# Kernel tuning notes

Measured on AMD Instinct MI355X. Metric: run time of the kernel, lower is better.

The kernel has to match this reference:

```python
import jax, jax.numpy as jnp
import numpy as np

B, N, T, D, H, L, N_HOP = 8, 512, 64, 256, 256, 2, 1
NEG = -1e18


def setup_inputs() -> dict:
    key = jax.random.key(0)
    ks = jax.random.split(key, 16)
    sc = 0.05
    return {
        "attn_mem": jax.random.normal(ks[0], (B, N, D), jnp.float32),
        "mem_sizes": jax.random.randint(ks[1], (B,), 1, N + 1).astype(jnp.int32),
        "lstm_in": jax.random.normal(ks[2], (B, T, D), jnp.float32),
        "init_h": jax.random.uniform(ks[3], (L, H), jnp.float32, -0.01, 0.01),
        "init_c": jax.random.uniform(ks[4], (L, H), jnp.float32, -0.01, 0.01),
        "init_i": jax.random.uniform(ks[5], (D,), jnp.float32, -0.1, 0.1),
        # stacked LSTM weights (layer0 input dim D == H so stacking is valid)
        "w_ih": jax.random.normal(ks[6], (L, 4 * H, D), jnp.float32) * sc,
        "w_hh": jax.random.normal(ks[7], (L, 4 * H, H), jnp.float32) * sc,
        "b_ih": jnp.zeros((L, 4 * H), jnp.float32),
        "b_hh": jnp.zeros((L, 4 * H), jnp.float32),
        "attn_wm": jax.random.normal(ks[8], (D, H), jnp.float32) * sc,
        "attn_wq": jax.random.normal(ks[9], (H, H), jnp.float32) * sc,
        "attn_v": jax.random.uniform(ks[10], (H,), jnp.float32, -0.01, 0.01),
        "hop_wm": jax.random.normal(ks[11], (D, H), jnp.float32) * sc,
        "hop_wq": jax.random.normal(ks[12], (H, H), jnp.float32) * sc,
        "hop_v": jax.random.uniform(ks[13], (H,), jnp.float32, -0.01, 0.01),
    }


def _additive_score(feat, query, v, wq):
    # feat: [B,N,H]  query: [B,S,H]  ->  score: [B,S,N]
    q = query @ wq  # [B,S,H]
    s = jnp.tanh(feat[:, None, :, :] + q[:, :, None, :])  # [B,S,N,H] (large)
    return jnp.einsum("bsnh,h->bsn", s, v)


def _run_lstm(x, h0, c0, w_ih, w_hh, b_ih, b_hh):
    # x: [S,B,D] time-major; PyTorch gate order i,f,g,o
    n_layer = h0.shape[0]

    def step(carry, x_t):
        h, c = carry
        inp = x_t
        hs, cs = [], []
        for l in range(n_layer):
            g = inp @ w_ih[l].T + h[l] @ w_hh[l].T + b_ih[l] + b_hh[l]
            i_g, f_g, g_g, o_g = jnp.split(g, 4, axis=-1)
            c_n = jax.nn.sigmoid(f_g) * c[l] + jax.nn.sigmoid(i_g) * jnp.tanh(g_g)
            h_n = jax.nn.sigmoid(o_g) * jnp.tanh(c_n)
            hs.append(h_n)
            cs.append(c_n)
            inp = h_n
        return (jnp.stack(hs), jnp.stack(cs)), inp

    _, ys = jax.lax.scan(step, (h0, c0), x)
    return ys  # [S,B,H]


def reference(attn_mem, mem_sizes, lstm_in, init_h, init_c, init_i,
              w_ih, w_hh, b_ih, b_hh,
              attn_wm, attn_wq, attn_v, hop_wm, hop_wq, hop_v):
    bs, n_mem, _ = attn_mem.shape
    attn_feat = attn_mem @ attn_wm  # [B,N,H]
    hop_feat = attn_mem @ hop_wm    # [B,N,H]

    h0 = jnp.broadcast_to(init_h[:, None, :], (init_h.shape[0], bs, init_h.shape[1]))
    c0 = jnp.broadcast_to(init_c[:, None, :], h0.shape)
    seq = jnp.concatenate(
        [jnp.broadcast_to(init_i[None, None, :], (bs, 1, init_i.shape[0])), lstm_in],
        axis=1,
    )  # [B,T+1,D]
    query = _run_lstm(seq.transpose(1, 0, 2), h0, c0, w_ih, w_hh, b_ih, b_hh)
    query = query.transpose(1, 0, 2)  # [B,T+1,H]

    valid = jnp.arange(n_mem)[None, None, :] < mem_sizes[:, None, None]  # [B,1,N]
    for _ in range(N_HOP):
        score = _additive_score(hop_feat, query, hop_v, hop_wq)  # [B,T+1,N]
        score = jnp.where(valid, score, NEG)
        norm = jax.nn.softmax(score, axis=-1)
        query = jnp.einsum("bsn,bnh->bsh", norm, hop_feat)

    return _additive_score(attn_feat, query, attn_v, attn_wq)  # [B,T+1,N]
```

## Files before the change

### kernel.cpp

```cpp
#include <hip/hip_runtime.h>

#define BB 8
#define NN 512
#define TT 64
#define SS 65
#define DD 256
#define HH 256
#define G4 1024

__device__ __forceinline__ float fsigmoid(float x) {
    return __builtin_amdgcn_rcpf(1.f + __expf(-x));
}
__device__ __forceinline__ float ftanh(float x) {
    float e = __expf(2.f * x);
    return fmaf(-2.f, __builtin_amdgcn_rcpf(e + 1.f), 1.f);
}

__global__ void __launch_bounds__(256) pre_kernel(
    const float* __restrict__ lstm_in, const float* __restrict__ init_i,
    const float* __restrict__ init_h, const float* __restrict__ w_ih,
    const float* __restrict__ b_ih, const float* __restrict__ b_hh,
    float* __restrict__ xg0,
    const float* __restrict__ attn_mem, const float* __restrict__ attn_wm,
    const float* __restrict__ hop_wm,
    float* __restrict__ attn_feat, float* __restrict__ hop_feat,
    unsigned long long* __restrict__ S0, unsigned long long* __restrict__ S1)
{
    const int tid = threadIdx.x;
    const int blk = blockIdx.x;
    if (blk >= 400) {
        int i = (blk - 400) * 256 + tid;
        if (i < 2048) {
            S0[i] = (1ULL << 32) | (unsigned long long)(unsigned)__float_as_uint(init_h[i & 255]);
        } else if (i < 4096) {
            S1[i - 2048] = (1ULL << 32)
                         | (unsigned long long)(unsigned)__float_as_uint(init_h[HH + (i & 255)]);
        } else if (i < 4096 + 65 * 2048) {
            S0[2048 + (i - 4096)] = 0ULL;
        } else if (i < 4096 + 130 * 2048) {
            S1[2048 + (i - (4096 + 65 * 2048))] = 0ULL;
        }
        return;
    }
    __shared__ __align__(16) float smem[3264];
    const int tm = (tid >> 4) * 4, tn = (tid & 15) * 4;
    const int arow = tid >> 2, akq = (tid & 3) << 2;

    if (blk < 144) {
        float* As = smem;
        float* Bs = smem + 1088;
        const int bm = (blk % 9) * 64, bn = (blk / 9) * 64;
        float acc[4][4] = {};
        for (int k0 = 0; k0 < 256; k0 += 16) {
            {
                int m = bm + arow;
                float4 v = make_float4(0.f, 0.f, 0.f, 0.f);
                if (m < 520) {
                    int s = m % 65, b = m / 65;
                    const float* src = (s == 0) ? (init_i + k0 + akq)
                        : (lstm_in + ((size_t)b * TT + (s - 1)) * DD + k0 + akq);
                    v = *(const float4*)src;
                }
                As[(akq + 0) * 68 + arow] = v.x; As[(akq + 1) * 68 + arow] = v.y;
                As[(akq + 2) * 68 + arow] = v.z; As[(akq + 3) * 68 + arow] = v.w;
            }
            {
                int n = bn + arow;
                float4 v = *(const float4*)(w_ih + (size_t)n * 256 + k0 + akq);
                Bs[(akq + 0) * 68 + (n - bn)] = v.x; Bs[(akq + 1) * 68 + (n - bn)] = v.y;
                Bs[(akq + 2) * 68 + (n - bn)] = v.z; Bs[(akq + 3) * 68 + (n - bn)] = v.w;
            }
            __syncthreads();
#pragma unroll
            for (int kk = 0; kk < 16; ++kk) {
                float4 a = *(const float4*)&As[kk * 68 + tm];
                float4 b = *(const float4*)&Bs[kk * 68 + tn];
                float av[4] = {a.x, a.y, a.z, a.w};
                float bv[4] = {b.x, b.y, b.z, b.w};
#pragma unroll
                for (int i = 0; i < 4; ++i)
#pragma unroll
                    for (int jj = 0; jj < 4; ++jj)
                        acc[i][jj] = fmaf(av[i], bv[jj], acc[i][jj]);
            }
            __syncthreads();
        }
        float bad[4];
#pragma unroll
        for (int jj = 0; jj < 4; ++jj)
            bad[jj] = b_ih[bn + tn + jj] + b_hh[bn + tn + jj];
#pragma unroll
        for (int i = 0; i < 4; ++i) {
            int m = bm + tm + i;
            if (m < 520)
                *(float4*)(xg0 + (size_t)m * 1024 + bn + tn) =
                    make_float4(acc[i][0] + bad[0], acc[i][1] + bad[1],
                                acc[i][2] + bad[2], acc[i][3] + bad[3]);
        }
    } else {
        float* As  = smem;
        float* Bs  = smem + 1088;
        float* Bs2 = smem + 2176;
        const int tileid = blk - 144;
        const int bm = (tileid & 63) * 64, bn = (tileid >> 6) * 64;
        float acc1[4][4] = {}, acc2[4][4] = {};
        for (int k0 = 0; k0 < 256; k0 += 16) {
            float4 va = *(const float4*)(attn_mem + (size_t)(bm + arow) * 256 + k0 + akq);
            As[(akq + 0) * 68 + arow] = va.x; As[(akq + 1) * 68 + arow] = va.y;
            As[(akq + 2) * 68 + arow] = va.z; As[(akq + 3) * 68 + arow] = va.w;
            int kk = tid >> 4, nq = (tid & 15) << 2;
            *(float4*)&Bs[kk * 68 + nq]  = *(const float4*)(attn_wm + (size_t)(k0 + kk) * 256 + bn + nq);
            *(float4*)&Bs2[kk * 68 + nq] = *(const float4*)(hop_wm  + (size_t)(k0 + kk) * 256 + bn + nq);
            __syncthreads();
#pragma unroll
            for (int kk2 = 0; kk2 < 16; ++kk2) {
                float4 a  = *(const float4*)&As[kk2 * 68 + tm];
                float4 b1 = *(const float4*)&Bs[kk2 * 68 + tn];
                float4 b2 = *(const float4*)&Bs2[kk2 * 68 + tn];
                float av[4] = {a.x, a.y, a.z, a.w};
                float b1v[4] = {b1.x, b1.y, b1.z, b1.w};
                float b2v[4] = {b2.x, b2.y, b2.z, b2.w};
#pragma unroll
                for (int i = 0; i < 4; ++i)
#pragma unroll
                    for (int jj = 0; jj < 4; ++jj) {
                        acc1[i][jj] = fmaf(av[i], b1v[jj], acc1[i][jj]);
                        acc2[i][jj] = fmaf(av[i], b2v[jj], acc2[i][jj]);
                    }
            }
            __syncthreads();
        }
#pragma unroll
        for (int i = 0; i < 4; ++i) {
            int m = bm + tm + i;
            *(float4*)(attn_feat + (size_t)m * 256 + bn + tn) =
                make_float4(acc1[i][0], acc1[i][1], acc1[i][2], acc1[i][3]);
            *(float4*)(hop_feat + (size_t)m * 256 + bn + tn) =
                make_float4(acc2[i][0], acc2[i][1], acc2[i][2], acc2[i][3]);
        }
    }
}

__device__ __forceinline__ float dot16(const float4* w, const float* hp) {
    float4 s = make_float4(0.f, 0.f, 0.f, 0.f);
#pragma unroll
    for (int k = 0; k < 16; ++k) {
        float4 h4 = *(const float4*)(hp + 4 * k);
        s.x = fmaf(w[k].x, h4.x, s.x);
        s.y = fmaf(w[k].y, h4.y, s.y);
        s.z = fmaf(w[k].z, h4.z, s.z);
        s.w = fmaf(w[k].w, h4.w, s.w);
    }
    return (s.x + s.y) + (s.z + s.w);
}

__device__ __forceinline__ float poll_h(const unsigned long long* p, unsigned want) {
    unsigned long long u = __hip_atomic_load(p, __ATOMIC_RELAXED, __HIP_MEMORY_SCOPE_AGENT);
    while ((unsigned)(u >> 32) != want) {
        u = __hip_atomic_load(p, __ATOMIC_RELAXED, __HIP_MEMORY_SCOPE_AGENT);
    }
    return __uint_as_float((unsigned)u);
}

__global__ void __launch_bounds__(1024, 4) lstm_kernel(
    const float* __restrict__ w_ih, const float* __restrict__ w_hh,
    const float* __restrict__ b_ih, const float* __restrict__ b_hh,
    const float* __restrict__ xg0, const float* __restrict__ init_c,
    unsigned long long* __restrict__ S0, unsigned long long* __restrict__ S1,
    float* __restrict__ query)
{
    __shared__ float hls[64 * 68];
    __shared__ float part[1024];
    const int tid = threadIdx.x;
    const int blk = blockIdx.x;
    const int g = tid * 2;
    const int sb = g >> 8, r0 = g & 255, sg0 = r0 >> 6, kq = r0 & 63;
    float* const dst = &hls[(sg0 * 8 + sb) * 68 + kq];

    if (blk < 32) {
        const int jl = tid & 7, gate = (tid >> 3) & 3, b = (tid >> 5) & 7, seg = tid >> 8;
        const int j0 = blk * 8, j = j0 + jl;
        float4 w[16];
        {
            const float4* wr = (const float4*)(w_hh + (size_t)(gate * HH + j) * HH + seg * 64);
#pragma unroll
            for (int k = 0; k < 16; ++k) w[k] = wr[k];
        }
        const int fj = tid >> 3, fb = tid & 7;
        float creg = (tid < 64) ? init_c[j0 + fj] : 0.f;
        const int chunk = seg * 8 + b;
        const int pidx = (chunk * 8 + jl) * 4 + gate;

        for (int t = 0; t < SS; ++t) {
            float xg[4];
            if (tid < 64) {
                const float* xp = xg0 + ((size_t)fb * SS + t) * G4 + (j0 + fj);
#pragma unroll
                for (int gg = 0; gg < 4; ++gg) xg[gg] = xp[gg * 256];
            }
            {
                const unsigned long long* src = S0 + (size_t)t * 2048 + g;
                dst[0] = poll_h(src, (unsigned)(t + 1));
                dst[1] = poll_h(src + 1, (unsigned)(t + 1));
            }
            __syncthreads();
            part[pidx] = dot16(w, &hls[chunk * 68]);
            __syncthreads();
            if (tid < 64) {
                float g0 = xg[0], g1 = xg[1], g2 = xg[2], g3 = xg[3];
#pragma unroll
                for (int s2 = 0; s2 < 4; ++s2) {
                    const float* pp = &part[((s2 * 8 + fb) * 8 + fj) * 4];
                    g0 += pp[0]; g1 += pp[1]; g2 += pp[2]; g3 += pp[3];
                }
                float c = fsigmoid(g1) * creg + fsigmoid(g0) * ftanh(g2);
                float h = fsigmoid(g3) * ftanh(c);
                creg = c;
                unsigned long long u = ((unsigned long long)(unsigned)(t + 2) << 32)
                                     | (unsigned long long)(unsigned)__float_as_uint(h);
                __hip_atomic_store(S0 + (size_t)(t + 1) * 2048 + fb * 256 + (j0 + fj), u,
                                   __ATOMIC_RELAXED, __HIP_MEMORY_SCOPE_AGENT);
            }
        }
    } else {
        const int jl = tid & 3, gate = (tid >> 2) & 3, b = (tid >> 4) & 7, seg = tid >> 7;
        const int j0 = (blk - 32) * 4, j = j0 + jl;
        float4 w[16];
        {
            const float* base = (seg < 4)
                ? (w_ih + (size_t)(G4 + gate * HH + j) * HH + seg * 64)
                : (w_hh + (size_t)(G4 + gate * HH + j) * HH + (seg - 4) * 64);
            const float4* wr = (const float4*)base;
#pragma unroll
            for (int k = 0; k < 16; ++k) w[k] = wr[k];
        }
        const int fj = tid >> 3, fb = tid & 7;
        float creg = 0.f, bias[4] = {0.f, 0.f, 0.f, 0.f};
        if (tid < 32) {
            creg = init_c[HH + j0 + fj];
#pragma unroll
            for (int gg = 0; gg < 4; ++gg)
                bias[gg] = b_ih[G4 + gg * HH + j0 + fj] + b_hh[G4 + gg * HH + j0 + fj];
        }
        const int chunk = seg * 8 + b;
        const int pidx = chunk * 16 + jl * 4 + gate;

        for (int t = 0; t < SS; ++t) {
            {
                const unsigned long long* src = S0 + (size_t)(t + 1) * 2048 + g;
                dst[0] = poll_h(src, (unsigned)(t + 2));
                dst[1] = poll_h(src + 1, (unsigned)(t + 2));
            }
            __syncthreads();
            if (seg < 4) part[pidx] = dot16(w, &hls[chunk * 68]);
            {
                const unsigned long long* src = S1 + (size_t)t * 2048 + g;
                float v0 = poll_h(src, (unsigned)(t + 1));
                float v1 = poll_h(src + 1, (unsigned)(t + 1));
                dst[32 * 68 + 0] = v0;
                dst[32 * 68 + 1] = v1;
            }
            __syncthreads();
            if (seg >= 4) part[pidx] = dot16(w, &hls[chunk * 68]);
            __syncthreads();
            if (tid < 32) {
                float g0 = bias[0], g1 = bias[1], g2 = bias[2], g3 = bias[3];
#pragma unroll
                for (int s2 = 0; s2 < 8; ++s2) {
                    const float* pp = &part[(s2 * 8 + fb) * 16 + fj * 4];
                    g0 += pp[0]; g1 += pp[1]; g2 += pp[2]; g3 += pp[3];
                }
                float c = fsigmoid(g1) * creg + fsigmoid(g0) * ftanh(g2);
                float h = fsigmoid(g3) * ftanh(c);
                creg = c;
                int jj = j0 + fj;
                unsigned long long u = ((unsigned long long)(unsigned)(t + 2) << 32)
                                     | (unsigned long long)(unsigned)__float_as_uint(h);
                __hip_atomic_store(S1 + (size_t)(t + 1) * 2048 + fb * 256 + jj, u,
                                   __ATOMIC_RELAXED, __HIP_MEMORY_SCOPE_AGENT);
                query[((size_t)fb * SS + t) * HH + jj] = h;
            }
        }
    }
}

__global__ void __launch_bounds__(512) score_kernel(
    const float* __restrict__ qin, const float* __restrict__ wq,
    const float* __restrict__ feat, const float* __restrict__ v,
    const int* __restrict__ mem_sizes, float* __restrict__ out, int masked)
{
    const int s = blockIdx.x, b = blockIdx.y, tid = threadIdx.x;
    __shared__ float qrow[256], vs[256];
    __shared__ float partm[512];
    if (tid < 256) qrow[tid] = qin[((size_t)b * SS + s) * HH + tid];
    else           vs[tid - 256] = v[tid - 256];
    __syncthreads();
    {
        const int kh = tid >> 8, hp2 = tid & 255;
        const float* wp = wq + (size_t)(kh * 128) * HH + hp2;
        const float* qr = qrow + kh * 128;
        float a = 0.f;
#pragma unroll 8
        for (int hh = 0; hh < 128; ++hh) a = fmaf(qr[hh], wp[(size_t)hh * HH], a);
        partm[tid] = a;
    }
    __syncthreads();
    if (tid < 256) qrow[tid] = partm[tid] + partm[tid + 256];
    __syncthreads();

    const int msize = masked ? mem_sizes[b] : NN;
    const int lane = tid & 63, wv = tid >> 6;
    float* ob = out + ((size_t)b * SS + s) * NN;
    for (int n = msize + tid; n < NN; n += 512) ob[n] = -1e18f;
    float4 q4 = *(const float4*)&qrow[lane << 2];
    float4 v4 = *(const float4*)&vs[lane << 2];
    const float* fb = feat + (size_t)b * NN * HH + (lane << 2);
    int n = wv;
    for (; n + 8 < msize; n += 16) {
        float4 fa = *(const float4*)(fb + (size_t)n * HH);
        float4 fc = *(const float4*)(fb + (size_t)(n + 8) * HH);
        float a0 = ftanh(fa.x + q4.x) * v4.x + ftanh(fa.y + q4.y) * v4.y
                 + ftanh(fa.z + q4.z) * v4.z + ftanh(fa.w + q4.w) * v4.w;
        float a1 = ftanh(fc.x + q4.x) * v4.x + ftanh(fc.y + q4.y) * v4.y
                 + ftanh(fc.z + q4.z) * v4.z + ftanh(fc.w + q4.w) * v4.w;
#pragma unroll
        for (int off = 32; off; off >>= 1) {
            a0 += __shfl_xor(a0, off, 64);
            a1 += __shfl_xor(a1, off, 64);
        }
        if (lane == 0) { ob[n] = a0; ob[n + 8] = a1; }
    }
    for (; n < msize; n += 8) {
        float4 fa = *(const float4*)(fb + (size_t)n * HH);
        float a0 = ftanh(fa.x + q4.x) * v4.x + ftanh(fa.y + q4.y) * v4.y
                 + ftanh(fa.z + q4.z) * v4.z + ftanh(fa.w + q4.w) * v4.w;
#pragma unroll
        for (int off = 32; off; off >>= 1) a0 += __shfl_xor(a0, off, 64);
        if (lane == 0) ob[n] = a0;
    }
}

__global__ void __launch_bounds__(512) swsum8_kernel(
    const float* __restrict__ sc, const float* __restrict__ feat,
    const int* __restrict__ mem_sizes, float* __restrict__ q2raw)
{
    const int st = blockIdx.x, b = blockIdx.y, tid = threadIdx.x;
    const int s0 = st * 5;
    const int msize = mem_sizes[b];
    __shared__ float pls[5 * 520];
    __shared__ float partw[8 * 5 * 256];
    for (int i = tid; i < 5 * 512; i += 512) {
        int s = i >> 9, n = i & 511;
        pls[s * 520 + n] = (n < msize)
            ? sc[((size_t)b * SS + s0 + s) * NN + n] : -3e38f;
    }
    __syncthreads();
    const int lane = tid & 63, wv = tid >> 6;
    if (wv < 5) {
        const int r = wv;
        float x[8];
        float m = -3e38f;
#pragma unroll
        for (int k = 0; k < 8; ++k) {
            x[k] = pls[r * 520 + lane + 64 * k];
            m = fmaxf(m, x[k]);
        }
#pragma unroll
        for (int off = 32; off; off >>= 1) m = fmaxf(m, __shfl_xor(m, off, 64));
        float l = 0.f;
#pragma unroll
        for (int k = 0; k < 8; ++k) { x[k] = __expf(x[k] - m); l += x[k]; }
#pragma unroll
        for (int off = 32; off; off >>= 1) l += __shfl_xor(l, off, 64);
        float inv = __builtin_amdgcn_rcpf(l);
#pragma unroll
        for (int k = 0; k < 8; ++k) pls[r * 520 + lane + 64 * k] = x[k] * inv;
    }
    __syncthreads();
    {
        float4 acc[5];
#pragma unroll
        for (int s = 0; s < 5; ++s) acc[s] = make_float4(0.f, 0.f, 0.f, 0.f);
        const float* fb = feat + (size_t)b * NN * HH + (lane << 2);
        const int nb = wv * 64;
        for (int i = 0; i < 64; ++i) {
            float4 f = *(const float4*)(fb + (size_t)(nb + i) * HH);
#pragma unroll
            for (int s = 0; s < 5; ++s) {
                float p = pls[s * 520 + nb + i];
                acc[s].x = fmaf(p, f.x, acc[s].x);
                acc[s].y = fmaf(p, f.y, acc[s].y);
                acc[s].z = fmaf(p, f.z, acc[s].z);
                acc[s].w = fmaf(p, f.w, acc[s].w);
            }
        }
#pragma unroll
        for (int s = 0; s < 5; ++s)
            *(float4*)&partw[(wv * 5 + s) * 256 + (lane << 2)] = acc[s];
    }
    __syncthreads();
    for (int i = tid; i < 5 * 256; i += 512) {
        int s = i >> 8, h = i & 255;
        float r = 0.f;
#pragma unroll
        for (int w = 0; w < 8; ++w) r += partw[(w * 5 + s) * 256 + h];
        q2raw[((size_t)b * SS + s0 + s) * HH + h] = r;
    }
}

extern "C" void kernel_launch(void* const* d_in, const int* in_sizes, int n_in,
                              void* d_out, int out_size, void* d_ws, size_t ws_size,
                              hipStream_t stream) {
    const float* attn_mem  = (const float*)d_in[0];
    const int*   mem_sizes = (const int*)d_in[1];
    const float* lstm_in   = (const float*)d_in[2];
    const float* init_h    = (const float*)d_in[3];
    const float* init_c    = (const float*)d_in[4];
    const float* init_i    = (const float*)d_in[5];
    const float* w_ih      = (const float*)d_in[6];
    const float* w_hh      = (const float*)d_in[7];
    const float* b_ih      = (const float*)d_in[8];
    const float* b_hh      = (const float*)d_in[9];
    const float* attn_wm   = (const float*)d_in[10];
    const float* attn_wq   = (const float*)d_in[11];
    const float* attn_v    = (const float*)d_in[12];
    const float* hop_wm    = (const float*)d_in[13];
    const float* hop_wq    = (const float*)d_in[14];
    const float* hop_v     = (const float*)d_in[15];
    float* out = (float*)d_out;

    float* ws        = (float*)d_ws;
    float* attn_feat = ws;
    float* hop_feat  = ws + 1048576;
    float* xg0       = ws + 2097152;
    float* query     = ws + 2629632;
    float* region    = ws + 2762752;
    unsigned long long* S0 = (unsigned long long*)region;
    unsigned long long* S1 = (unsigned long long*)(region + 270336);
    float* sc     = region;
    float* q2raw  = region + 266240;

    pre_kernel<<<1456, 256, 0, stream>>>(lstm_in, init_i, init_h, w_ih, b_ih, b_hh,
                                         xg0, attn_mem, attn_wm, hop_wm,
                                         attn_feat, hop_feat, S0, S1);
    {
        void* args[] = { (void*)&w_ih, (void*)&w_hh, (void*)&b_ih, (void*)&b_hh,
                         (void*)&xg0, (void*)&init_c, (void*)&S0, (void*)&S1,
                         (void*)&query };
        hipLaunchCooperativeKernel(lstm_kernel, dim3(96), dim3(1024), args, 0u, stream);
    }
    score_kernel<<<dim3(65, 8), 512, 0, stream>>>(query, hop_wq, hop_feat, hop_v,
                                                  mem_sizes, sc, 1);
    swsum8_kernel<<<dim3(13, 8), 512, 0, stream>>>(sc, hop_feat, mem_sizes, q2raw);
    score_kernel<<<dim3(65, 8), 512, 0, stream>>>(q2raw, attn_wq, attn_feat, attn_v,
                                                  mem_sizes, out, 0);
}
```

Before: 285.7 us.

## Remap LSTM recurrent dot products to 16-lane segments with shuffle reductions

Restructures the persistent LSTM kernel's per-step matvec. Each thread now holds 16 weights (4 float4) and computes 4 batch dot products over a 16-element slice. Partial sums are reduced with wavefront xor-shuffles instead of a large shared partial-sum array, and hidden state is stored in shared memory with an XOR swizzle to avoid bank conflicts. Layer 1 now waits on both its inputs before a single barrier rather than overlapping its two halves. This cuts register pressure and shared-memory reduction work on the serial critical path. In exchange it adds shuffle latency and removes the split-phase overlap in layer 1.

```diff
diff --git a/kernel.cpp b/kernel.cpp
--- a/kernel.cpp
+++ b/kernel.cpp
@@ -141,19 +141,6 @@
     }
 }
 
-__device__ __forceinline__ float dot16(const float4* w, const float* hp) {
-    float4 s = make_float4(0.f, 0.f, 0.f, 0.f);
-#pragma unroll
-    for (int k = 0; k < 16; ++k) {
-        float4 h4 = *(const float4*)(hp + 4 * k);
-        s.x = fmaf(w[k].x, h4.x, s.x);
-        s.y = fmaf(w[k].y, h4.y, s.y);
-        s.z = fmaf(w[k].z, h4.z, s.z);
-        s.w = fmaf(w[k].w, h4.w, s.w);
-    }
-    return (s.x + s.y) + (s.z + s.w);
-}
-
 __device__ __forceinline__ float poll_h(const unsigned long long* p, unsigned want) {
     unsigned long long u = __hip_atomic_load(p, __ATOMIC_RELAXED, __HIP_MEMORY_SCOPE_AGENT);
     while ((unsigned)(u >> 32) != want) {
@@ -169,27 +156,31 @@
     unsigned long long* __restrict__ S0, unsigned long long* __restrict__ S1,
     float* __restrict__ query)
 {
-    __shared__ float hls[64 * 68];
-    __shared__ float part[1024];
+    __shared__ __align__(16) float hls0[8 * 260];
+    __shared__ __align__(16) float hls1[8 * 260];
+    __shared__ float part[256];
     const int tid = threadIdx.x;
     const int blk = blockIdx.x;
-    const int g = tid * 2;
-    const int sb = g >> 8, r0 = g & 255, sg0 = r0 >> 6, kq = r0 & 63;
-    float* const dst = &hls[(sg0 * 8 + sb) * 68 + kq];
+    const int seg = tid & 15;
+    const int row = (tid >> 4) & 31;
+    const int bp  = tid >> 9;
+    const int xr  = (seg >> 2) & 3;
+    const int g   = tid * 2;
+    const int b_s = g >> 8, k_s = g & 255;
+    const int k_p = k_s ^ (((k_s >> 6) & 3) << 2);
+    const int fj = tid >> 3, fb = tid & 7;
 
     if (blk < 32) {
-        const int jl = tid & 7, gate = (tid >> 3) & 3, b = (tid >> 5) & 7, seg = tid >> 8;
-        const int j0 = blk * 8, j = j0 + jl;
-        float4 w[16];
-        {
-            const float4* wr = (const float4*)(w_hh + (size_t)(gate * HH + j) * HH + seg * 64);
-#pragma unroll
-            for (int k = 0; k < 16; ++k) w[k] = wr[k];
-        }
-        const int fj = tid >> 3, fb = tid & 7;
+        const int j0 = blk * 8;
+        const int gate = row >> 3, jl = row & 7;
+        const float4* wf4 = (const float4*)(w_hh + (size_t)(gate * HH + j0 + jl) * HH);
+        float4 w0 = wf4[seg * 4 + 0], w1 = wf4[seg * 4 + 1];
+        float4 w2 = wf4[seg * 4 + 2], w3 = wf4[seg * 4 + 3];
+        float* const dst = &hls0[b_s * 260 + k_p];
+        const float* hb[4];
+#pragma unroll
+        for (int i = 0; i < 4; ++i) hb[i] = &hls0[(bp * 4 + i) * 260];
         float creg = (tid < 64) ? init_c[j0 + fj] : 0.f;
-        const int chunk = seg * 8 + b;
-        const int pidx = (chunk * 8 + jl) * 4 + gate;
 
         for (int t = 0; t < SS; ++t) {
             float xg[4];
@@ -204,17 +195,37 @@
                 dst[1] = poll_h(src + 1, (unsigned)(t + 1));
             }
             __syncthreads();
-            part[pidx] = dot16(w, &hls[chunk * 68]);
+            float p[4] = {0.f, 0.f, 0.f, 0.f};
+#pragma unroll
+            for (int c = 0; c < 4; ++c) {
+                float4 w4 = (c == 0) ? w0 : (c == 1) ? w1 : (c == 2) ? w2 : w3;
+                const int cs = (seg * 4 + (c ^ xr)) * 4;
+#pragma unroll
+                for (int i = 0; i < 4; ++i) {
+                    float4 h4 = *(const float4*)(hb[i] + cs);
+                    p[i] = fmaf(w4.x, h4.x, p[i]);
+                    p[i] = fmaf(w4.y, h4.y, p[i]);
+                    p[i] = fmaf(w4.z, h4.z, p[i]);
+                    p[i] = fmaf(w4.w, h4.w, p[i]);
+                }
+            }
+#pragma unroll
+            for (int i = 0; i < 4; ++i) {
+                p[i] += __shfl_xor(p[i], 1, 64);
+                p[i] += __shfl_xor(p[i], 2, 64);
+                p[i] += __shfl_xor(p[i], 4, 64);
+                p[i] += __shfl_xor(p[i], 8, 64);
+            }
+            if (seg == 0)
+                *(float4*)&part[row * 8 + bp * 4] = make_float4(p[0], p[1], p[2], p[3]);
             __syncthreads();
             if (tid < 64) {
-                float g0 = xg[0], g1 = xg[1], g2 = xg[2], g3 = xg[3];
-#pragma unroll
-                for (int s2 = 0; s2 < 4; ++s2) {
-                    const float* pp = &part[((s2 * 8 + fb) * 8 + fj) * 4];
-                    g0 += pp[0]; g1 += pp[1]; g2 += pp[2]; g3 += pp[3];
-                }
-                float c = fsigmoid(g1) * creg + fsigmoid(g0) * ftanh(g2);
-                float h = fsigmoid(g3) * ftanh(c);
+                float gv[4];
+#pragma unroll
+                for (int gg = 0; gg < 4; ++gg)
+                    gv[gg] = xg[gg] + part[(gg * 8 + fj) * 8 + fb];
+                float c = fsigmoid(gv[1]) * creg + fsigmoid(gv[0]) * ftanh(gv[2]);
+                float h = fsigmoid(gv[3]) * ftanh(c);
                 creg = c;
                 unsigned long long u = ((unsigned long long)(unsigned)(t + 2) << 32)
                                      | (unsigned long long)(unsigned)__float_as_uint(h);
@@ -223,18 +234,18 @@
             }
         }
     } else {
-        const int jl = tid & 3, gate = (tid >> 2) & 3, b = (tid >> 4) & 7, seg = tid >> 7;
-        const int j0 = (blk - 32) * 4, j = j0 + jl;
-        float4 w[16];
-        {
-            const float* base = (seg < 4)
-                ? (w_ih + (size_t)(G4 + gate * HH + j) * HH + seg * 64)
-                : (w_hh + (size_t)(G4 + gate * HH + j) * HH + (seg - 4) * 64);
-            const float4* wr = (const float4*)base;
-#pragma unroll
-            for (int k = 0; k < 16; ++k) w[k] = wr[k];
-        }
-        const int fj = tid >> 3, fb = tid & 7;
+        const int j0 = (blk - 32) * 4;
+        const int mat = row >> 4, gate = (row >> 2) & 3, jl = row & 3;
+        const float* wbase = mat ? w_hh : w_ih;
+        const float4* wf4 = (const float4*)(wbase + (size_t)(G4 + gate * HH + j0 + jl) * HH);
+        float4 w0 = wf4[seg * 4 + 0], w1 = wf4[seg * 4 + 1];
+        float4 w2 = wf4[seg * 4 + 2], w3 = wf4[seg * 4 + 3];
+        float* const dst0 = &hls0[b_s * 260 + k_p];
+        float* const dst1 = &hls1[b_s * 260 + k_p];
+        const float* hsrc = mat ? hls1 : hls0;
+        const float* hb[4];
+#pragma unroll
+        for (int i = 0; i < 4; ++i) hb[i] = &hsrc[(bp * 4 + i) * 260];
         float creg = 0.f, bias[4] = {0.f, 0.f, 0.f, 0.f};
         if (tid < 32) {
             creg = init_c[HH + j0 + fj];
@@ -242,36 +253,51 @@
             for (int gg = 0; gg < 4; ++gg)
                 bias[gg] = b_ih[G4 + gg * HH + j0 + fj] + b_hh[G4 + gg * HH + j0 + fj];
         }
-        const int chunk = seg * 8 + b;
-        const int pidx = chunk * 16 + jl * 4 + gate;
 
         for (int t = 0; t < SS; ++t) {
             {
+                const unsigned long long* src = S1 + (size_t)t * 2048 + g;
+                dst1[0] = poll_h(src, (unsigned)(t + 1));
+                dst1[1] = poll_h(src + 1, (unsigned)(t + 1));
+            }
+            {
                 const unsigned long long* src = S0 + (size_t)(t + 1) * 2048 + g;
-                dst[0] = poll_h(src, (unsigned)(t + 2));
-                dst[1] = poll_h(src + 1, (unsigned)(t + 2));
-            }
-            __syncthreads();
-            if (seg < 4) part[pidx] = dot16(w, &hls[chunk * 68]);
-            {
-                const unsigned long long* src = S1 + (size_t)t * 2048 + g;
-                float v0 = poll_h(src, (unsigned)(t + 1));
-                float v1 = poll_h(src + 1, (unsigned)(t + 1));
-                dst[32 * 68 + 0] = v0;
-                dst[32 * 68 + 1] = v1;
-            }
-            __syncthreads();
-            if (seg >= 4) part[pidx] = dot16(w, &hls[chunk * 68]);
+                dst0[0] = poll_h(src, (unsigned)(t + 2));
+                dst0[1] = poll_h(src + 1, (unsigned)(t + 2));
+            }
+            __syncthreads();
+            float p[4] = {0.f, 0.f, 0.f, 0.f};
+#pragma unroll
+            for (int c = 0; c < 4; ++c) {
+                float4 w4 = (c == 0) ? w0 : (c == 1) ? w1 : (c == 2) ? w2 : w3;
+                const int cs = (seg * 4 + (c ^ xr)) * 4;
+#pragma unroll
+                for (int i = 0; i < 4; ++i) {
+                    float4 h4 = *(const float4*)(hb[i] + cs);
+                    p[i] = fmaf(w4.x, h4.x, p[i]);
+                    p[i] = fmaf(w4.y, h4.y, p[i]);
+                    p[i] = fmaf(w4.z, h4.z, p[i]);
+                    p[i] = fmaf(w4.w, h4.w, p[i]);
+                }
+            }
+#pragma unroll
+            for (int i = 0; i < 4; ++i) {
+                p[i] += __shfl_xor(p[i], 1, 64);
+                p[i] += __shfl_xor(p[i], 2, 64);
+                p[i] += __shfl_xor(p[i], 4, 64);
+                p[i] += __shfl_xor(p[i], 8, 64);
+            }
+            if (seg == 0)
+                *(float4*)&part[row * 8 + bp * 4] = make_float4(p[0], p[1], p[2], p[3]);
             __syncthreads();
             if (tid < 32) {
-                float g0 = bias[0], g1 = bias[1], g2 = bias[2], g3 = bias[3];
-#pragma unroll
-                for (int s2 = 0; s2 < 8; ++s2) {
-                    const float* pp = &part[(s2 * 8 + fb) * 16 + fj * 4];
-                    g0 += pp[0]; g1 += pp[1]; g2 += pp[2]; g3 += pp[3];
-                }
-                float c = fsigmoid(g1) * creg + fsigmoid(g0) * ftanh(g2);
-                float h = fsigmoid(g3) * ftanh(c);
+                float gv[4];
+#pragma unroll
+                for (int gg = 0; gg < 4; ++gg)
+                    gv[gg] = bias[gg] + part[(gg * 4 + fj) * 8 + fb]
+                                      + part[(16 + gg * 4 + fj) * 8 + fb];
+                float c = fsigmoid(gv[1]) * creg + fsigmoid(gv[0]) * ftanh(gv[2]);
+                float h = fsigmoid(gv[3]) * ftanh(c);
                 creg = c;
                 int jj = j0 + fj;
                 unsigned long long u = ((unsigned long long)(unsigned)(t + 2) << 32)
```

New measurement: 358.0 us. +25.3%, slower.
